# Kernel optimization log

Hardware: AMD Instinct MI355X
Metric: run time of the kernel (lower is better)

Reference implementation:

```python
import jax, jax.numpy as jnp
import numpy as np

N = 50000          # number of nodes / output rows (len(degs))
IN_C, OUT_C = 16, 16
EDGE_F = 13        # edge feature dim fed to filter net
HID = 32           # filter-net hidden width
E_NOMINAL = 800000 # target number of edges (sum of degs)


def setup_inputs() -> dict:
    rng = np.random.default_rng(0)
    # variable per-node degrees in [0, 32], adjusted so they sum exactly to E_NOMINAL
    degs = rng.integers(0, 33, size=N).astype(np.int64)
    degs[0] = max(0, degs[0] + (E_NOMINAL - int(degs.sum())))
    E = int(degs.sum())
    # segment id of each edge = destination node (equivalent to the degs-driven loop)
    idxd = np.repeat(np.arange(N, dtype=np.int32), degs)
    idxn = rng.integers(0, N, size=E).astype(np.int32)  # source node gather index

    key = jax.random.key(0)
    k1, k2, k3, k4 = jax.random.split(key, 4)
    x = jax.random.normal(k1, (N, IN_C), jnp.float32)
    edgefeats = jax.random.normal(k2, (E, EDGE_F), jnp.float32)
    # filter net: Linear(EDGE_F->HID) -> ReLU -> Linear(HID->IN_C*OUT_C)
    W1 = jax.random.normal(k3, (EDGE_F, HID), jnp.float32) / np.float32(np.sqrt(EDGE_F))
    b1 = jnp.zeros((HID,), jnp.float32)
    W2 = jax.random.normal(k4, (HID, IN_C * OUT_C), jnp.float32) / np.float32(np.sqrt(HID))
    b2 = jnp.zeros((IN_C * OUT_C,), jnp.float32)
    return {
        "x": x, "edgefeats": edgefeats,
        "W1": W1, "b1": b1, "W2": W2, "b2": b2,
        "idxn": jnp.asarray(idxn), "idxd": jnp.asarray(idxd),
        "degs": jnp.asarray(degs.astype(np.float32)),
    }


def reference(x, edgefeats, W1, b1, W2, b2, idxn, idxd, degs):
    # filter net generates a per-edge [IN_C, OUT_C] weight matrix
    h = jax.nn.relu(edgefeats @ W1 + b1)                 # [E, HID]
    w = (h @ W2 + b2).reshape(-1, IN_C, OUT_C)           # [E, IN_C, OUT_C]
    # gather source-node features and apply per-edge matvec (bmm with [E,1,IN_C])
    sel = x[idxn]                                        # [E, IN_C]
    prod = jnp.einsum('ei,eio->eo', sel, w)              # [E, OUT_C]
    # segment-mean over each node's incoming edges; degree-0 nodes -> 0
    s = jax.ops.segment_sum(prod, idxd, num_segments=N)  # [N, OUT_C]
    d = degs[:, None]
    return jnp.where(d > 0, s / jnp.maximum(d, 1.0), jnp.float32(0.0))
```

## Files before the change

kernel.cpp:

```cpp
#include <hip/hip_runtime.h>

typedef _Float16 half2v __attribute__((ext_vector_type(2)));
typedef _Float16 half4v __attribute__((ext_vector_type(4)));
typedef _Float16 half8v __attribute__((ext_vector_type(8)));
typedef float   float4v __attribute__((ext_vector_type(4)));

#define INC     16
#define OUTC    16
#define EFN     13
#define HIDC    32
#define EPB     512
#define NTILES  (EPB / 16)
#define MAXSPAN 80

#define GLOBAL_AS __attribute__((address_space(1)))
#define LDS_AS    __attribute__((address_space(3)))

union H8 { half8v v; half2v h2[4]; };

#define SB(t, l, j) (((t) * 64 + (l)) * 8 + (j))

__global__ __launch_bounds__(256) void pack_w2(const float* __restrict__ W2,
                                               _Float16* __restrict__ wsB)
{
    const int i = blockIdx.x * 256 + threadIdx.x;
    const int j = i & 7;
    const int l = (i >> 3) & 63;
    const int t = i >> 9;
    const int q = l >> 4, n = l & 15;
    const int kk = (j < 4) ? (q * 4 + j) : (16 + q * 4 + (j & 3));
    wsB[i] = (_Float16)W2[kk * 256 + t * 16 + n];
}

__global__ __launch_bounds__(256) void edge_kernel(
    const float* __restrict__ x,
    const float* __restrict__ edgefeats,
    const float* __restrict__ W1,
    const float* __restrict__ b1,
    const float* __restrict__ b2,
    const int*   __restrict__ idxn,
    const int*   __restrict__ idxd,
    const float* __restrict__ degs,
    const _Float16* __restrict__ wsB,
    float*       __restrict__ out,
    float*       __restrict__ wsPfirst,
    float*       __restrict__ wsPlast,
    int*         __restrict__ wsMeta,
    int E)
{
    __shared__ __align__(16) _Float16 sB[16 * 64 * 8];
    __shared__ float         lacc[MAXSPAN * OUTC];
    __shared__ int           sidxn[EPB];
    __shared__ __align__(4) unsigned char su[EPB];

    const int tid  = threadIdx.x;
    const int lane = tid & 63;
    const int wid  = tid >> 6;
    const int n    = lane & 15;
    const int q    = lane >> 4;

    const long b0   = (long)blockIdx.x * EPB;
    const long bEnd = (b0 + EPB < (long)E) ? (b0 + EPB) : (long)E;
    const int  d_lo = idxd[b0];
    const int  d_hi = idxd[bEnd - 1];
    const int  span = d_hi - d_lo;

    #pragma unroll
    for (int it = 0; it < 4; ++it) {
        const int chunk = wid + it * 4;
        __builtin_amdgcn_global_load_lds(
            (const GLOBAL_AS unsigned int*)((const char*)wsB + chunk * 1024 + lane * 16),
            (LDS_AS unsigned int*)((char*)sB + chunk * 1024),
            16, 0, 0);
    }

    #pragma unroll
    for (int it = 0; it < MAXSPAN * OUTC / 256; ++it) lacc[tid + it * 256] = 0.0f;
    {
        const int i2 = tid * 2;
        long e0 = b0 + i2, e1 = b0 + i2 + 1;
        if (e0 >= (long)E) e0 = E - 1;
        if (e1 >= (long)E) e1 = E - 1;
        sidxn[i2]     = idxn[e0];
        sidxn[i2 + 1] = idxn[e1];
        const unsigned u0 = (unsigned)(idxd[e0] - d_lo);
        const unsigned u1 = (unsigned)(idxd[e1] - d_lo);
        *(unsigned short*)&su[i2] = (unsigned short)(u0 | (u1 << 8));
    }

    half4v a1, a2;
    float4v c1, c2;
    #pragma unroll
    for (int jj = 0; jj < 4; ++jj) {
        const int f = q * 4 + jj;
        const bool ok = (f < EFN);
        a1[jj] = ok ? (_Float16)W1[f * HIDC + n]      : (_Float16)0.f;
        a2[jj] = ok ? (_Float16)W1[f * HIDC + 16 + n] : (_Float16)0.f;
        c1[jj] = b1[q * 4 + jj];
        c2[jj] = b1[16 + q * 4 + jj];
    }
    half8v bfragB2;
    #pragma unroll
    for (int j = 0; j < 8; ++j) {
        _Float16 val = (_Float16)0.f;
        if (q < 2) val = (_Float16)b2[(q * 8 + j) * 16 + n];
        bfragB2[j] = val;
    }

    const int f0 = (q < 3) ? (q * 4) : 9;

    __syncthreads();

    for (int t16 = wid; t16 < NTILES; t16 += 4) {
        const long base = b0 + (long)t16 * 16;
        const long eM   = base + n;
        const bool vM   = (eM < (long)E);
        const long eMc  = vM ? eM : (long)(E - 1);

        const unsigned u4  = *(const unsigned*)&su[t16 * 16 + q * 4];
        const int      node = sidxn[t16 * 16 + n];

        const float4 ef4 = *(const float4*)(edgefeats + (size_t)eMc * EFN + f0);

        const float4* xp = (const float4*)(x + (size_t)node * INC);
        float4 s0 = xp[0], s1 = xp[1], s2 = xp[2], s3 = xp[3];
        if (!vM) { s0 = make_float4(0,0,0,0); s1 = s0; s2 = s0; s3 = s0; }

        half2v selh[8];
        { half2v t = {(_Float16)s0.x, (_Float16)s0.y}; selh[0] = t; }
        { half2v t = {(_Float16)s0.z, (_Float16)s0.w}; selh[1] = t; }
        { half2v t = {(_Float16)s1.x, (_Float16)s1.y}; selh[2] = t; }
        { half2v t = {(_Float16)s1.z, (_Float16)s1.w}; selh[3] = t; }
        { half2v t = {(_Float16)s2.x, (_Float16)s2.y}; selh[4] = t; }
        { half2v t = {(_Float16)s2.z, (_Float16)s2.w}; selh[5] = t; }
        { half2v t = {(_Float16)s3.x, (_Float16)s3.y}; selh[6] = t; }
        { half2v t = {(_Float16)s3.z, (_Float16)s3.w}; selh[7] = t; }

        half4v efB;
        if (q < 3) {
            efB[0] = (_Float16)ef4.x; efB[1] = (_Float16)ef4.y;
            efB[2] = (_Float16)ef4.z; efB[3] = (_Float16)ef4.w;
        } else {
            efB[0] = (_Float16)ef4.w; efB[1] = (_Float16)0.f;
            efB[2] = (_Float16)0.f;   efB[3] = (_Float16)0.f;
        }

        const float4v hf1 = __builtin_amdgcn_mfma_f32_16x16x16f16(a1, efB, c1, 0, 0, 0);
        const float4v hf2 = __builtin_amdgcn_mfma_f32_16x16x16f16(a2, efB, c2, 0, 0, 0);

        H8 hu;
        #pragma unroll
        for (int r = 0; r < 2; ++r) {
            half2v t1 = {(_Float16)fmaxf(hf1[2*r], 0.f), (_Float16)fmaxf(hf1[2*r+1], 0.f)};
            half2v t2 = {(_Float16)fmaxf(hf2[2*r], 0.f), (_Float16)fmaxf(hf2[2*r+1], 0.f)};
            hu.h2[r]     = t1;
            hu.h2[2 + r] = t2;
        }

        float4v acc = {0.f, 0.f, 0.f, 0.f};
        #pragma unroll
        for (int t = 0; t < 16; ++t) {
            _Float16 sv = (t & 1) ? selh[t >> 1][1] : selh[t >> 1][0];
            half2v sb = {sv, sv};
            H8 a;
            a.h2[0] = sb * hu.h2[0];
            a.h2[1] = sb * hu.h2[1];
            a.h2[2] = sb * hu.h2[2];
            a.h2[3] = sb * hu.h2[3];
            const half8v bf = *(const half8v*)&sB[SB(t, lane, 0)];
            acc = __builtin_amdgcn_mfma_f32_16x16x32_f16(a.v, bf, acc, 0, 0, 0);
        }
        {
            H8 a;
            #pragma unroll
            for (int j2 = 0; j2 < 4; ++j2) {
                half2v zz = {(_Float16)0.f, (_Float16)0.f};
                a.h2[j2] = (q < 2) ? selh[q * 4 + j2] : zz;
            }
            acc = __builtin_amdgcn_mfma_f32_16x16x32_f16(a.v, bfragB2, acc, 0, 0, 0);
        }

        const unsigned rep = (u4 & 0xffu) * 0x01010101u;
        if (u4 == rep) {
            atomicAdd(&lacc[(u4 & 0xffu) * OUTC + n],
                      acc[0] + acc[1] + acc[2] + acc[3]);
        } else {
            #pragma unroll
            for (int r = 0; r < 4; ++r)
                atomicAdd(&lacc[((u4 >> (8 * r)) & 0xffu) * OUTC + n], acc[r]);
        }
    }

    __syncthreads();

    const bool first_starts = (b0 == 0)        || (idxd[b0 - 1] != d_lo);
    const bool last_ends    = (bEnd == (long)E) || (idxd[bEnd]   != d_hi);

    for (int i = tid; i < (span + 1) * OUTC; i += 256) {
        const int u = i >> 4;
        const int o = i & 15;
        const int v = d_lo + u;
        const float bin = lacc[u * OUTC + o];
        const bool starts = (u > 0)    || first_starts;
        const bool ends   = (u < span) || last_ends;
        if (starts && ends) {
            const float dg = degs[v];
            out[(size_t)v * OUTC + o] = (dg > 0.0f) ? bin / dg : 0.0f;
        } else if (!starts) {
            wsPfirst[(size_t)blockIdx.x * OUTC + o] = bin;
        } else {
            wsPlast[(size_t)blockIdx.x * OUTC + o] = bin;
        }
    }
    if (tid == 0) {
        wsMeta[blockIdx.x * 4 + 0] = d_hi;
        wsMeta[blockIdx.x * 4 + 1] = last_ends ? 1 : 0;
        wsMeta[blockIdx.x * 4 + 2] =
            (((span > 0) || first_starts) && !last_ends) ? 1 : 0;
    }
}

__global__ __launch_bounds__(256) void fixup_kernel(
    const float* __restrict__ degs,
    float*       __restrict__ out,
    const float* __restrict__ wsPfirst,
    const float* __restrict__ wsPlast,
    const int*   __restrict__ wsMeta,
    int N, int nblocks)
{
    const int t = blockIdx.x * 256 + threadIdx.x;

    if (t < nblocks && wsMeta[t * 4 + 2]) {
        const int v = wsMeta[t * 4 + 0];
        float tot[OUTC];
        #pragma unroll
        for (int o = 0; o < OUTC; ++o) tot[o] = wsPlast[(size_t)t * OUTC + o];
        for (int j = t + 1; j < nblocks; ++j) {
            #pragma unroll
            for (int o = 0; o < OUTC; ++o) tot[o] += wsPfirst[(size_t)j * OUTC + o];
            if (wsMeta[j * 4 + 0] != v || wsMeta[j * 4 + 1]) break;
        }
        const float dg = degs[v];
        #pragma unroll
        for (int o = 0; o < OUTC; ++o) out[(size_t)v * OUTC + o] = tot[o] / dg;
    }

    if (t < N && degs[t] == 0.0f) {
        float4* op = (float4*)(out + (size_t)t * OUTC);
        const float4 z = make_float4(0, 0, 0, 0);
        op[0] = z; op[1] = z; op[2] = z; op[3] = z;
    }
}

extern "C" void kernel_launch(void* const* d_in, const int* in_sizes, int n_in,
                              void* d_out, int out_size, void* d_ws, size_t ws_size,
                              hipStream_t stream)
{
    const float* x         = (const float*)d_in[0];
    const float* edgefeats = (const float*)d_in[1];
    const float* W1        = (const float*)d_in[2];
    const float* b1        = (const float*)d_in[3];
    const float* W2        = (const float*)d_in[4];
    const float* b2        = (const float*)d_in[5];
    const int*   idxn      = (const int*)d_in[6];
    const int*   idxd      = (const int*)d_in[7];
    const float* degs      = (const float*)d_in[8];

    const int E = in_sizes[6];
    const int N = in_sizes[8];
    const int nblocks = (E + EPB - 1) / EPB;

    _Float16* wsB    = (_Float16*)d_ws;
    float* wsPfirst  = (float*)((char*)d_ws + 16384);
    float* wsPlast   = wsPfirst + (size_t)nblocks * OUTC;
    int*   wsMeta    = (int*)(wsPlast + (size_t)nblocks * OUTC);

    pack_w2<<<32, 256, 0, stream>>>(W2, wsB);

    edge_kernel<<<nblocks, 256, 0, stream>>>(x, edgefeats, W1, b1, b2,
                                             idxn, idxd, degs, wsB, (float*)d_out,
                                             wsPfirst, wsPlast, wsMeta, E);

    const int fthreads = (N > nblocks) ? N : nblocks;
    fixup_kernel<<<(fthreads + 255) / 256, 256, 0, stream>>>(
        degs, (float*)d_out, wsPfirst, wsPlast, wsMeta, N, nblocks);
}
```

Before: 161.3 us.

## Use single-wave blocks with W2 fragments held in registers

Restructures the edge kernel from 256-thread blocks over 512 edges to 64-thread single-wavefront blocks over 128 edges. Each lane keeps all 16 packed W2 B-fragments in registers instead of staging them in LDS, and the source-node index for the next tile is prefetched from global memory instead of being staged in shared memory. This removes LDS B-fragment reads in the inner MFMA loop and shrinks the LDS footprint. In exchange it increases register pressure, reloads W2 per block with four times as many blocks, and produces more boundary partials for the fixup pass. MAXSPAN stays sized for the larger tile.

```diff
diff --git a/kernel.cpp b/kernel.cpp
--- a/kernel.cpp
+++ b/kernel.cpp
@@ -9,16 +9,11 @@
 #define OUTC    16
 #define EFN     13
 #define HIDC    32
-#define EPB     512
+#define EPB     128
 #define NTILES  (EPB / 16)
 #define MAXSPAN 80
 
-#define GLOBAL_AS __attribute__((address_space(1)))
-#define LDS_AS    __attribute__((address_space(3)))
-
 union H8 { half8v v; half2v h2[4]; };
-
-#define SB(t, l, j) (((t) * 64 + (l)) * 8 + (j))
 
 __global__ __launch_bounds__(256) void pack_w2(const float* __restrict__ W2,
                                                _Float16* __restrict__ wsB)
@@ -32,7 +27,7 @@
     wsB[i] = (_Float16)W2[kk * 256 + t * 16 + n];
 }
 
-__global__ __launch_bounds__(256) void edge_kernel(
+__global__ __launch_bounds__(64, 3) void edge_kernel(
     const float* __restrict__ x,
     const float* __restrict__ edgefeats,
     const float* __restrict__ W1,
@@ -48,14 +43,10 @@
     int*         __restrict__ wsMeta,
     int E)
 {
-    __shared__ __align__(16) _Float16 sB[16 * 64 * 8];
-    __shared__ float         lacc[MAXSPAN * OUTC];
-    __shared__ int           sidxn[EPB];
+    __shared__ float lacc[MAXSPAN * OUTC];
     __shared__ __align__(4) unsigned char su[EPB];
 
-    const int tid  = threadIdx.x;
-    const int lane = tid & 63;
-    const int wid  = tid >> 6;
+    const int lane = threadIdx.x;
     const int n    = lane & 15;
     const int q    = lane >> 4;
 
@@ -65,24 +56,18 @@
     const int  d_hi = idxd[bEnd - 1];
     const int  span = d_hi - d_lo;
 
-    #pragma unroll
-    for (int it = 0; it < 4; ++it) {
-        const int chunk = wid + it * 4;
-        __builtin_amdgcn_global_load_lds(
-            (const GLOBAL_AS unsigned int*)((const char*)wsB + chunk * 1024 + lane * 16),
-            (LDS_AS unsigned int*)((char*)sB + chunk * 1024),
-            16, 0, 0);
-    }
-
-    #pragma unroll
-    for (int it = 0; it < MAXSPAN * OUTC / 256; ++it) lacc[tid + it * 256] = 0.0f;
+    H8 bfr[16];
+    #pragma unroll
+    for (int t = 0; t < 16; ++t)
+        bfr[t].v = *(const half8v*)(wsB + ((size_t)(t * 64 + lane) * 8));
+
+    #pragma unroll
+    for (int it = 0; it < MAXSPAN * OUTC / 64; ++it) lacc[lane + it * 64] = 0.0f;
     {
-        const int i2 = tid * 2;
+        const int i2 = lane * 2;
         long e0 = b0 + i2, e1 = b0 + i2 + 1;
         if (e0 >= (long)E) e0 = E - 1;
         if (e1 >= (long)E) e1 = E - 1;
-        sidxn[i2]     = idxn[e0];
-        sidxn[i2 + 1] = idxn[e1];
         const unsigned u0 = (unsigned)(idxd[e0] - d_lo);
         const unsigned u1 = (unsigned)(idxd[e1] - d_lo);
         *(unsigned short*)&su[i2] = (unsigned short)(u0 | (u1 << 8));
@@ -111,14 +96,23 @@
 
     __syncthreads();
 
-    for (int t16 = wid; t16 < NTILES; t16 += 4) {
+    const int ntile_blk = (int)((bEnd - b0 + 15) >> 4);
+    long e0n = b0 + n;
+    int nodeN = idxn[(e0n < (long)E) ? e0n : (long)(E - 1)];
+
+    for (int t16 = 0; t16 < ntile_blk; ++t16) {
         const long base = b0 + (long)t16 * 16;
         const long eM   = base + n;
         const bool vM   = (eM < (long)E);
         const long eMc  = vM ? eM : (long)(E - 1);
 
-        const unsigned u4  = *(const unsigned*)&su[t16 * 16 + q * 4];
-        const int      node = sidxn[t16 * 16 + n];
+        const int node = nodeN;
+        {
+            const long en = base + 16 + n;
+            nodeN = idxn[(en < (long)E) ? en : (long)(E - 1)];
+        }
+
+        const unsigned u4 = *(const unsigned*)&su[t16 * 16 + q * 4];
 
         const float4 ef4 = *(const float4*)(edgefeats + (size_t)eMc * EFN + f0);
 
@@ -167,8 +161,7 @@
             a.h2[1] = sb * hu.h2[1];
             a.h2[2] = sb * hu.h2[2];
             a.h2[3] = sb * hu.h2[3];
-            const half8v bf = *(const half8v*)&sB[SB(t, lane, 0)];
-            acc = __builtin_amdgcn_mfma_f32_16x16x32_f16(a.v, bf, acc, 0, 0, 0);
+            acc = __builtin_amdgcn_mfma_f32_16x16x32_f16(a.v, bfr[t].v, acc, 0, 0, 0);
         }
         {
             H8 a;
@@ -196,7 +189,7 @@
     const bool first_starts = (b0 == 0)        || (idxd[b0 - 1] != d_lo);
     const bool last_ends    = (bEnd == (long)E) || (idxd[bEnd]   != d_hi);
 
-    for (int i = tid; i < (span + 1) * OUTC; i += 256) {
+    for (int i = lane; i < (span + 1) * OUTC; i += 64) {
         const int u = i >> 4;
         const int o = i & 15;
         const int v = d_lo + u;
@@ -212,7 +205,7 @@
             wsPlast[(size_t)blockIdx.x * OUTC + o] = bin;
         }
     }
-    if (tid == 0) {
+    if (lane == 0) {
         wsMeta[blockIdx.x * 4 + 0] = d_hi;
         wsMeta[blockIdx.x * 4 + 1] = last_ends ? 1 : 0;
         wsMeta[blockIdx.x * 4 + 2] =
@@ -277,9 +270,9 @@
 
     pack_w2<<<32, 256, 0, stream>>>(W2, wsB);
 
-    edge_kernel<<<nblocks, 256, 0, stream>>>(x, edgefeats, W1, b1, b2,
-                                             idxn, idxd, degs, wsB, (float*)d_out,
-                                             wsPfirst, wsPlast, wsMeta, E);
+    edge_kernel<<<nblocks, 64, 0, stream>>>(x, edgefeats, W1, b1, b2,
+                                            idxn, idxd, degs, wsB, (float*)d_out,
+                                            wsPfirst, wsPlast, wsMeta, E);
 
     const int fthreads = (N > nblocks) ? N : nblocks;
     fixup_kernel<<<(fthreads + 255) / 256, 256, 0, stream>>>(
```

Measured after the change: 163.8 us. No clear change (+1.5%).
